# Kernel tuning notes

Measured on AMD Instinct MI355X. Metric: run time of the kernel, lower is better.

## Reference

```python
import jax, jax.numpy as jnp
import numpy as np

INPUT_SIZE = 16
K = 50
HIDDEN_COUNT = 25
FINAL_WIDTH = INPUT_SIZE + HIDDEN_COUNT * K  # 1266


def setup_inputs() -> dict:
    key = jax.random.key(0)
    k1, k2, k3, k4, k5 = jax.random.split(key, 5)
    B = 32768
    state = jax.random.normal(k1, (B, INPUT_SIZE), dtype=jnp.float32)
    # Zero-padded weight stack: layer i uses Ws[i, :, : INPUT_SIZE + i*K]
    Ws = jax.random.normal(k2, (HIDDEN_COUNT, K, FINAL_WIDTH), dtype=jnp.float32) * 0.05
    bs = jax.random.normal(k3, (HIDDEN_COUNT, K), dtype=jnp.float32) * 0.05
    Wout = jax.random.normal(k4, (FINAL_WIDTH, 1), dtype=jnp.float32) * 0.05
    bout = jax.random.normal(k5, (1,), dtype=jnp.float32) * 0.05
    return {"state": state, "Ws": Ws, "bs": bs, "Wout": Wout, "bout": bout}


def reference(state, Ws, bs, Wout, bout):
    x = state  # [B, 16], grows by 50 per layer
    for i in range(HIDDEN_COUNT):  # fixed-size structural loop over layers
        width = INPUT_SIZE + i * K
        w = Ws[i, :, :width]                       # [50, width] (static slice)
        y = jax.nn.leaky_relu(x @ w.T + bs[i], negative_slope=0.01)  # [B, 50]
        x = jnp.concatenate([x, y], axis=1)        # [B, width+50]
    return x @ Wout + bout  # [B, 1]
```

## Files before the change

### kernel.cpp

```cpp
#include <hip/hip_runtime.h>


#define IN 16
#define KJ 50
#define NL 25
#define FW 1266
#define TR 24
#define NB 1366
#define BTOT 32768
#define XSTR 1288
#define NTHREADS 512
#define XLO_OFF 61824
#define SLAB_OFF 123648
#define LDS_BYTES 156416
#define CHUNK_STRIDE 3200
#define TOTAL_CHUNKS 973

typedef __attribute__((ext_vector_type(8))) short bf16x8;
typedef __attribute__((ext_vector_type(16))) float f32x16;

__device__ __forceinline__ unsigned short bf16_hi(float x, float* hif) {
    unsigned u = __float_as_uint(x);
    unsigned h = (u + 0x8000u) >> 16;
    *hif = __uint_as_float(h << 16);
    return (unsigned short)h;
}
__device__ __forceinline__ unsigned short bf16_rnd(float x) {
    return (unsigned short)((__float_as_uint(x) + 0x8000u) >> 16);
}

__device__ __forceinline__ void split8(const float* __restrict__ rowp, int kb, int width,
                                       unsigned hi[4], unsigned lo[4]) {
#pragma unroll
    for (int p = 0; p < 4; ++p) {
        unsigned h2[2], l2[2];
#pragma unroll
        for (int q = 0; q < 2; ++q) {
            int k = kb + p * 2 + q;
            float v = (k < width) ? rowp[k] : 0.f;
            float hif;
            unsigned short h = bf16_hi(v, &hif);
            h2[q] = h;
            l2[q] = bf16_rnd(v - hif);
        }
        hi[p] = h2[0] | (h2[1] << 16);
        lo[p] = l2[0] | (l2[1] << 16);
    }
}

__global__ __launch_bounds__(64, 1) void split_w(const float* __restrict__ Ws,
                                                 char* __restrict__ wsbuf) {
    int rem = blockIdx.x, layer = 0;
    size_t off = 0;
    for (;;) {
        int c = (IN + KJ * layer + 15) >> 4;
        if (rem < c) break;
        rem -= c; off += (size_t)c * CHUNK_STRIDE; ++layer;
    }
    const int ci = rem, k0 = ci << 4, width = IN + KJ * layer;
    const float* Wl = Ws + (size_t)layer * KJ * FW;
    char* base = wsbuf + off + (size_t)ci * CHUNK_STRIDE;
    const int l = threadIdx.x, ll = l & 31, kh = l >> 5;
    const int kb = k0 + kh * 8;

    unsigned hi[4], lo[4];
    split8(Wl + (size_t)ll * FW, kb, width, hi, lo);
    *reinterpret_cast<uint4*>(base + l * 16)        = make_uint4(hi[0], hi[1], hi[2], hi[3]);
    *reinterpret_cast<uint4*>(base + 1024 + l * 16) = make_uint4(lo[0], lo[1], lo[2], lo[3]);
    if (ll < 18) {
        split8(Wl + (size_t)(32 + ll) * FW, kb, width, hi, lo);
        *reinterpret_cast<uint4*>(base + 2048 + (kh * 18 + ll) * 16) = make_uint4(hi[0], hi[1], hi[2], hi[3]);
        *reinterpret_cast<uint4*>(base + 2624 + (kh * 18 + ll) * 16) = make_uint4(lo[0], lo[1], lo[2], lo[3]);
    }
}

__global__ __launch_bounds__(NTHREADS, 1) void densenet_mfma(
    const float* __restrict__ state, const char* __restrict__ wsbuf,
    const float* __restrict__ bs,    const float* __restrict__ Wout,
    const float* __restrict__ bout,  float* __restrict__ out)
{
    __shared__ __align__(16) char lds[LDS_BYTES];
    unsigned short* xhi = (unsigned short*)lds;
    unsigned short* xlo = (unsigned short*)(lds + XLO_OFF);
    float* slab = (float*)(lds + SLAB_OFF);

    const int tid = threadIdx.x;
    const int w   = tid >> 6;
    const int l   = tid & 63;
    const int ll  = l & 31, kh = l >> 5;
    const long row0 = (long)blockIdx.x * TR;

    {
        unsigned* p = (unsigned*)lds;
        for (int i = tid; i < (XLO_OFF * 2) / 4; i += NTHREADS) p[i] = 0u;
    }
    __syncthreads();
    if (tid < TR * IN) {
        int r = tid >> 4, c = tid & 15;
        if (row0 + r < BTOT) {
            float v = state[(row0 + r) * IN + c];
            float hif;
            xhi[r * XSTR + c] = bf16_hi(v, &hif);
            xlo[r * XSTR + c] = bf16_rnd(v - hif);
        }
    }

    int width = IN;
    size_t wofs = 0;
    for (int layer = 0; layer < NL; ++layer) {
        const int chunks = (width + 15) >> 4;
        f32x16 acc0, acc1;
#pragma unroll
        for (int i = 0; i < 16; ++i) { acc0[i] = 0.f; acc1[i] = 0.f; }

        __syncthreads();

        const char* wb = wsbuf + wofs;
        for (int ci = w; ci < chunks; ci += 8) {
            const char* cb = wb + (size_t)ci * CHUNK_STRIDE;
            const int kof = (ci << 4) + (kh << 3);
            bf16x8 ah = *(const bf16x8*)&xhi[ll * XSTR + kof];
            bf16x8 al = *(const bf16x8*)&xlo[ll * XSTR + kof];
            bf16x8 bh0 = *(const bf16x8*)(cb + l * 16);
            bf16x8 bl0 = *(const bf16x8*)(cb + 1024 + l * 16);
            bf16x8 bh1 = {0,0,0,0,0,0,0,0}, bl1 = {0,0,0,0,0,0,0,0};
            if (ll < 18) {
                bh1 = *(const bf16x8*)(cb + 2048 + (kh * 18 + ll) * 16);
                bl1 = *(const bf16x8*)(cb + 2624 + (kh * 18 + ll) * 16);
            }
            acc0 = __builtin_amdgcn_mfma_f32_32x32x16_bf16(al, bh0, acc0, 0, 0, 0);
            acc0 = __builtin_amdgcn_mfma_f32_32x32x16_bf16(ah, bl0, acc0, 0, 0, 0);
            acc0 = __builtin_amdgcn_mfma_f32_32x32x16_bf16(ah, bh0, acc0, 0, 0, 0);
            acc1 = __builtin_amdgcn_mfma_f32_32x32x16_bf16(al, bh1, acc1, 0, 0, 0);
            acc1 = __builtin_amdgcn_mfma_f32_32x32x16_bf16(ah, bl1, acc1, 0, 0, 0);
            acc1 = __builtin_amdgcn_mfma_f32_32x32x16_bf16(ah, bh1, acc1, 0, 0, 0);
        }

#pragma unroll
        for (int r = 0; r < 8; ++r) {
            slab[w * 1024 + (0 * 8 + r) * 64 + l] = acc0[r];
            slab[w * 1024 + (1 * 8 + r) * 64 + l] = acc1[r];
        }
        __syncthreads();
        for (int idx = tid; idx < 16 * KJ; idx += NTHREADS) {
            int row = idx / KJ, j = idx % KJ;
            int n = j >> 5;
            int lj = (j & 31) | (((row >> 2) & 1) << 5);
            int r = (row & 3) | ((row >> 3) << 2);
            float s = 0.f;
#pragma unroll
            for (int q = 0; q < 8; ++q) s += slab[q * 1024 + (n * 8 + r) * 64 + lj];
            s += bs[layer * KJ + j];
            s = (s > 0.f) ? s : 0.01f * s;
            float hif;
            xhi[row * XSTR + width + j] = bf16_hi(s, &hif);
            xlo[row * XSTR + width + j] = bf16_rnd(s - hif);
        }
        __syncthreads();
#pragma unroll
        for (int r = 0; r < 4; ++r) {
            slab[w * 512 + (0 * 4 + r) * 64 + l] = acc0[8 + r];
            slab[w * 512 + (1 * 4 + r) * 64 + l] = acc1[8 + r];
        }
        __syncthreads();
        for (int idx = tid; idx < 8 * KJ; idx += NTHREADS) {
            int row = idx / KJ + 16, j = idx % KJ;
            int n = j >> 5;
            int lj = (j & 31) | (((row >> 2) & 1) << 5);
            int r = row & 3;
            float s = 0.f;
#pragma unroll
            for (int q = 0; q < 8; ++q) s += slab[q * 512 + (n * 4 + r) * 64 + lj];
            s += bs[layer * KJ + j];
            s = (s > 0.f) ? s : 0.01f * s;
            float hif;
            xhi[row * XSTR + width + j] = bf16_hi(s, &hif);
            xlo[row * XSTR + width + j] = bf16_rnd(s - hif);
        }
        width += KJ;
        wofs += (size_t)chunks * CHUNK_STRIDE;
    }

    __syncthreads();
#pragma unroll
    for (int rr = 0; rr < 3; ++rr) {
        const int row = w * 3 + rr;
        const long grow = row0 + row;
        float s = 0.f;
        for (int k = l; k < FW; k += 64) {
            float xv = __uint_as_float((unsigned)xhi[row * XSTR + k] << 16)
                     + __uint_as_float((unsigned)xlo[row * XSTR + k] << 16);
            s += xv * Wout[k];
        }
#pragma unroll
        for (int m = 32; m >= 1; m >>= 1) s += __shfl_xor(s, m, 64);
        if (l == 0 && grow < BTOT) out[grow] = s + bout[0];
    }
}

extern "C" void kernel_launch(void* const* d_in, const int* in_sizes, int n_in,
                              void* d_out, int out_size, void* d_ws, size_t ws_size,
                              hipStream_t stream) {
    const float* state = (const float*)d_in[0];
    const float* Ws    = (const float*)d_in[1];
    const float* bs    = (const float*)d_in[2];
    const float* Wout  = (const float*)d_in[3];
    const float* bout  = (const float*)d_in[4];
    float* out = (float*)d_out;
    char* wsbuf = (char*)d_ws;

    split_w<<<dim3(TOTAL_CHUNKS), dim3(64), 0, stream>>>(Ws, wsbuf);
    densenet_mfma<<<dim3(NB), dim3(NTHREADS), 0, stream>>>(state, wsbuf, bs, Wout, bout, out);
}
```

Measured before the change: 535.3 us.

## Split waves across output column halves and K quarters with prefetched B loads

Waves now partition work by output-column half (n) and K-chunk quarter (kq), so each wave keeps a single accumulator instead of two. B fragments are double-buffered from global memory one step ahead. The cross-wave reduction now sums 4 partial slabs instead of 8 and runs in one pass with two barriers per layer instead of four. The aim is fewer barriers, less LDS reduction traffic and better latency hiding, in exchange for issuing twice as many A loads from LDS per chunk across waves.

```diff
diff --git a/kernel.cpp b/kernel.cpp
--- a/kernel.cpp
+++ b/kernel.cpp
@@ -12,7 +12,7 @@
 #define NTHREADS 512
 #define XLO_OFF 61824
 #define SLAB_OFF 123648
-#define LDS_BYTES 156416
+#define LDS_BYTES 148224
 #define CHUNK_STRIDE 3200
 #define TOTAL_CHUNKS 973
 
@@ -71,6 +71,22 @@
         split8(Wl + (size_t)(32 + ll) * FW, kb, width, hi, lo);
         *reinterpret_cast<uint4*>(base + 2048 + (kh * 18 + ll) * 16) = make_uint4(hi[0], hi[1], hi[2], hi[3]);
         *reinterpret_cast<uint4*>(base + 2624 + (kh * 18 + ll) * 16) = make_uint4(lo[0], lo[1], lo[2], lo[3]);
+    }
+}
+
+__device__ __forceinline__ void loadB(const char* __restrict__ wb, int ci, int n,
+                                      int l, int ll, int kh, bf16x8& bh, bf16x8& bl) {
+    const char* cb = wb + (size_t)ci * CHUNK_STRIDE;
+    if (n == 0) {
+        bh = *(const bf16x8*)(cb + l * 16);
+        bl = *(const bf16x8*)(cb + 1024 + l * 16);
+    } else {
+        bf16x8 z = {0, 0, 0, 0, 0, 0, 0, 0};
+        bh = z; bl = z;
+        if (ll < 18) {
+            bh = *(const bf16x8*)(cb + 2048 + (kh * 18 + ll) * 16);
+            bl = *(const bf16x8*)(cb + 2624 + (kh * 18 + ll) * 16);
+        }
     }
 }
 
@@ -88,6 +104,8 @@
     const int w   = tid >> 6;
     const int l   = tid & 63;
     const int ll  = l & 31, kh = l >> 5;
+    const int kq  = w & 3;
+    const int n   = w >> 2;
     const long row0 = (long)blockIdx.x * TR;
 
     {
@@ -104,84 +122,72 @@
             xlo[r * XSTR + c] = bf16_rnd(v - hif);
         }
     }
+    __syncthreads();
 
     int width = IN;
     size_t wofs = 0;
     for (int layer = 0; layer < NL; ++layer) {
         const int chunks = (width + 15) >> 4;
-        f32x16 acc0, acc1;
-#pragma unroll
-        for (int i = 0; i < 16; ++i) { acc0[i] = 0.f; acc1[i] = 0.f; }
-
+        const char* wb = wsbuf + wofs;
+
+        f32x16 acc;
+#pragma unroll
+        for (int i = 0; i < 16; ++i) acc[i] = 0.f;
+
+        bf16x8 h0 = {0,0,0,0,0,0,0,0}, l0v = h0, h1 = h0, l1v = h0;
+        if (kq < chunks)     loadB(wb, kq,     n, l, ll, kh, h0, l0v);
+        if (kq + 4 < chunks) loadB(wb, kq + 4, n, l, ll, kh, h1, l1v);
+        for (int ci = kq; ci < chunks; ci += 8) {
+            {
+                const int kof = (ci << 4) + (kh << 3);
+                bf16x8 ah = *(const bf16x8*)&xhi[ll * XSTR + kof];
+                bf16x8 al = *(const bf16x8*)&xlo[ll * XSTR + kof];
+                acc = __builtin_amdgcn_mfma_f32_32x32x16_bf16(al, h0, acc, 0, 0, 0);
+                acc = __builtin_amdgcn_mfma_f32_32x32x16_bf16(ah, l0v, acc, 0, 0, 0);
+                acc = __builtin_amdgcn_mfma_f32_32x32x16_bf16(ah, h0, acc, 0, 0, 0);
+            }
+            if (ci + 8 < chunks) loadB(wb, ci + 8, n, l, ll, kh, h0, l0v);
+            if (ci + 4 < chunks) {
+                const int kof = ((ci + 4) << 4) + (kh << 3);
+                bf16x8 ah = *(const bf16x8*)&xhi[ll * XSTR + kof];
+                bf16x8 al = *(const bf16x8*)&xlo[ll * XSTR + kof];
+                acc = __builtin_amdgcn_mfma_f32_32x32x16_bf16(al, h1, acc, 0, 0, 0);
+                acc = __builtin_amdgcn_mfma_f32_32x32x16_bf16(ah, l1v, acc, 0, 0, 0);
+                acc = __builtin_amdgcn_mfma_f32_32x32x16_bf16(ah, h1, acc, 0, 0, 0);
+                if (ci + 12 < chunks) loadB(wb, ci + 12, n, l, ll, kh, h1, l1v);
+            }
+        }
+
+        {
+            float* sl = slab + kq * 1536;
+#pragma unroll
+            for (int r = 0; r < 12; ++r) {
+                int crow = (r & 3) + 8 * (r >> 2) + 4 * kh;
+                sl[crow * 64 + n * 32 + ll] = acc[r];
+            }
+        }
         __syncthreads();
 
-        const char* wb = wsbuf + wofs;
-        for (int ci = w; ci < chunks; ci += 8) {
-            const char* cb = wb + (size_t)ci * CHUNK_STRIDE;
-            const int kof = (ci << 4) + (kh << 3);
-            bf16x8 ah = *(const bf16x8*)&xhi[ll * XSTR + kof];
-            bf16x8 al = *(const bf16x8*)&xlo[ll * XSTR + kof];
-            bf16x8 bh0 = *(const bf16x8*)(cb + l * 16);
-            bf16x8 bl0 = *(const bf16x8*)(cb + 1024 + l * 16);
-            bf16x8 bh1 = {0,0,0,0,0,0,0,0}, bl1 = {0,0,0,0,0,0,0,0};
-            if (ll < 18) {
-                bh1 = *(const bf16x8*)(cb + 2048 + (kh * 18 + ll) * 16);
-                bl1 = *(const bf16x8*)(cb + 2624 + (kh * 18 + ll) * 16);
-            }
-            acc0 = __builtin_amdgcn_mfma_f32_32x32x16_bf16(al, bh0, acc0, 0, 0, 0);
-            acc0 = __builtin_amdgcn_mfma_f32_32x32x16_bf16(ah, bl0, acc0, 0, 0, 0);
-            acc0 = __builtin_amdgcn_mfma_f32_32x32x16_bf16(ah, bh0, acc0, 0, 0, 0);
-            acc1 = __builtin_amdgcn_mfma_f32_32x32x16_bf16(al, bh1, acc1, 0, 0, 0);
-            acc1 = __builtin_amdgcn_mfma_f32_32x32x16_bf16(ah, bl1, acc1, 0, 0, 0);
-            acc1 = __builtin_amdgcn_mfma_f32_32x32x16_bf16(ah, bh1, acc1, 0, 0, 0);
-        }
-
-#pragma unroll
-        for (int r = 0; r < 8; ++r) {
-            slab[w * 1024 + (0 * 8 + r) * 64 + l] = acc0[r];
-            slab[w * 1024 + (1 * 8 + r) * 64 + l] = acc1[r];
+#pragma unroll
+        for (int it = 0; it < 3; ++it) {
+            int idx = it * NTHREADS + tid;
+            int row = idx >> 6, j = idx & 63;
+            float s = slab[row * 64 + j] + slab[1536 + row * 64 + j]
+                    + slab[3072 + row * 64 + j] + slab[4608 + row * 64 + j];
+            if (j < KJ) {
+                s += bs[layer * KJ + j];
+                s = (s > 0.f) ? s : 0.01f * s;
+                float hif;
+                xhi[row * XSTR + width + j] = bf16_hi(s, &hif);
+                xlo[row * XSTR + width + j] = bf16_rnd(s - hif);
+            }
         }
         __syncthreads();
-        for (int idx = tid; idx < 16 * KJ; idx += NTHREADS) {
-            int row = idx / KJ, j = idx % KJ;
-            int n = j >> 5;
-            int lj = (j & 31) | (((row >> 2) & 1) << 5);
-            int r = (row & 3) | ((row >> 3) << 2);
-            float s = 0.f;
-#pragma unroll
-            for (int q = 0; q < 8; ++q) s += slab[q * 1024 + (n * 8 + r) * 64 + lj];
-            s += bs[layer * KJ + j];
-            s = (s > 0.f) ? s : 0.01f * s;
-            float hif;
-            xhi[row * XSTR + width + j] = bf16_hi(s, &hif);
-            xlo[row * XSTR + width + j] = bf16_rnd(s - hif);
-        }
-        __syncthreads();
-#pragma unroll
-        for (int r = 0; r < 4; ++r) {
-            slab[w * 512 + (0 * 4 + r) * 64 + l] = acc0[8 + r];
-            slab[w * 512 + (1 * 4 + r) * 64 + l] = acc1[8 + r];
-        }
-        __syncthreads();
-        for (int idx = tid; idx < 8 * KJ; idx += NTHREADS) {
-            int row = idx / KJ + 16, j = idx % KJ;
-            int n = j >> 5;
-            int lj = (j & 31) | (((row >> 2) & 1) << 5);
-            int r = row & 3;
-            float s = 0.f;
-#pragma unroll
-            for (int q = 0; q < 8; ++q) s += slab[q * 512 + (n * 4 + r) * 64 + lj];
-            s += bs[layer * KJ + j];
-            s = (s > 0.f) ? s : 0.01f * s;
-            float hif;
-            xhi[row * XSTR + width + j] = bf16_hi(s, &hif);
-            xlo[row * XSTR + width + j] = bf16_rnd(s - hif);
-        }
+
         width += KJ;
         wofs += (size_t)chunks * CHUNK_STRIDE;
     }
 
-    __syncthreads();
 #pragma unroll
     for (int rr = 0; rr < 3; ++rr) {
         const int row = w * 3 + rr;
```

Measured after the change: 550.5 us. 1.03x slower.
